# Performance work log

Measured on AMD Instinct MI355X. Metric: run time of the kernel, lower is better.

The kernel has to match this reference:

```python
import jax, jax.numpy as jnp
import numpy as np

N_HEAD = 16
NEG_INF = -1e30


def sparsemax(z):
    # sparsemax over last axis (Martins & Astudillo 2016)
    d = z.shape[-1]
    z_sorted = -jnp.sort(-z, axis=-1)                      # descending
    z_cumsum = jnp.cumsum(z_sorted, axis=-1)
    k = jnp.arange(1, d + 1, dtype=z.dtype)
    support = (1.0 + k * z_sorted) > z_cumsum
    rho = jnp.sum(support, axis=-1, keepdims=True)         # int, >=1
    rho_idx = jnp.clip(rho - 1, 0, None).astype(jnp.int32)
    cs_at_rho = jnp.take_along_axis(z_cumsum, rho_idx, axis=-1)
    tau = (cs_at_rho - 1.0) / jnp.maximum(rho.astype(z.dtype), 1.0)
    return jnp.clip(z - tau, 0.0, None)


def setup_inputs() -> dict:
    key = jax.random.key(0)
    ks = jax.random.split(key, 5)
    B, T, C = 4, 2048, 1024
    x = jax.random.normal(ks[0], (B, T, C), dtype=jnp.float32)
    W_attn = jax.random.normal(ks[1], (C, 3 * C), dtype=jnp.float32) * (1.0 / np.sqrt(C))
    b_attn = jax.random.normal(ks[2], (3 * C,), dtype=jnp.float32) * 0.01
    W_proj = jax.random.normal(ks[3], (C, C), dtype=jnp.float32) * (1.0 / np.sqrt(C))
    b_proj = jax.random.normal(ks[4], (C,), dtype=jnp.float32) * 0.01
    return {"x": x, "W_attn": W_attn, "b_attn": b_attn, "W_proj": W_proj, "b_proj": b_proj}


def reference(x, W_attn, b_attn, W_proj, b_proj):
    B, T, C = x.shape
    H = N_HEAD
    D = C // H
    qkv = x @ W_attn + b_attn                               # [B,T,3C]
    q, k, v = jnp.split(qkv, 3, axis=-1)
    q = q.reshape(B, T, H, D).transpose(0, 2, 1, 3)         # [B,H,T,D]
    k = k.reshape(B, T, H, D).transpose(0, 2, 1, 3)
    v = v.reshape(B, T, H, D).transpose(0, 2, 1, 3)
    # sparsemax over head dim of K (mode xsa_sparsemax_k)
    k = sparsemax(k)
    att = jnp.einsum('bhqd,bhkd->bhqk', q, k) * (1.0 / np.sqrt(D))
    causal = jnp.tril(jnp.ones((T, T), dtype=bool))
    att = jnp.where(causal[None, None], att, NEG_INF)
    att = jax.nn.softmax(att, axis=-1)
    y = jnp.einsum('bhqk,bhkd->bhqd', att, v)               # [B,H,T,D]
    # XSA output correction: subtract projection of y onto normalized v
    v_norm = jnp.sqrt(jnp.sum(v * v, axis=-1, keepdims=True))
    v_hat = v / jnp.maximum(v_norm, 1e-12)
    proj_coef = jnp.sum(y * v_hat, axis=-1, keepdims=True)
    y = y - proj_coef * v_hat
    y = y.transpose(0, 2, 1, 3).reshape(B, T, C)
    return y @ W_proj + b_proj
```

## Files before the change

### kernel.cpp

```cpp
#include <hip/hip_runtime.h>
#include <math.h>

#define NB 4
#define NH 16
#define TT 2048
#define CC 1024
#define DD 64
#define MM (NB * TT)
#define BK 32

typedef __attribute__((ext_vector_type(8))) _Float16 half8;
typedef __attribute__((ext_vector_type(4))) _Float16 half4;
typedef __attribute__((ext_vector_type(4))) float floatx4;

__device__ __forceinline__ void gload16(const _Float16* g, _Float16* l) {
    auto gp = (const __attribute__((address_space(1))) void*)(uintptr_t)g;
    auto lp = (__attribute__((address_space(3))) void*)(uint32_t)(uintptr_t)l;
    __builtin_amdgcn_global_load_lds(gp, lp, 16, 0, 0);
}

__global__ __launch_bounds__(256) void split_x_kernel(
    const float* __restrict__ x, _Float16* __restrict__ xh,
    _Float16* __restrict__ xl)
{
    size_t i = ((size_t)blockIdx.x * 256 + threadIdx.x) * 4;
    float4 v = *(const float4*)&x[i];
    half4 h, l;
    h.x = (_Float16)v.x; l.x = (_Float16)(v.x - (float)h.x);
    h.y = (_Float16)v.y; l.y = (_Float16)(v.y - (float)h.y);
    h.z = (_Float16)v.z; l.z = (_Float16)(v.z - (float)h.z);
    h.w = (_Float16)v.w; l.w = (_Float16)(v.w - (float)h.w);
    *(half4*)&xh[i] = h;
    *(half4*)&xl[i] = l;
}

__global__ __launch_bounds__(256) void splitT_w_kernel(
    const float* __restrict__ W, _Float16* __restrict__ WhT,
    _Float16* __restrict__ WlT, int K, int N)
{
    __shared__ float Ls[64][65];
    const int bN = blockIdx.x * 64;
    const int bK = blockIdx.y * 64;
    const int tid = threadIdx.x;
    const int g = tid >> 4, c = tid & 15;

    #pragma unroll
    for (int u = 0; u < 4; u++) {
        int r = u * 16 + g;
        float4 v = *(const float4*)&W[(size_t)(bK + r) * N + bN + c * 4];
        Ls[r][c * 4 + 0] = v.x; Ls[r][c * 4 + 1] = v.y;
        Ls[r][c * 4 + 2] = v.z; Ls[r][c * 4 + 3] = v.w;
    }
    __syncthreads();
    #pragma unroll
    for (int u = 0; u < 4; u++) {
        int n = u * 16 + g;
        half4 h, l;
        float f;
        f = Ls[c * 4 + 0][n]; h.x = (_Float16)f; l.x = (_Float16)(f - (float)h.x);
        f = Ls[c * 4 + 1][n]; h.y = (_Float16)f; l.y = (_Float16)(f - (float)h.y);
        f = Ls[c * 4 + 2][n]; h.z = (_Float16)f; l.z = (_Float16)(f - (float)h.z);
        f = Ls[c * 4 + 3][n]; h.w = (_Float16)f; l.w = (_Float16)(f - (float)h.w);
        size_t o = (size_t)(bN + n) * K + bK + c * 4;
        *(half4*)&WhT[o] = h;
        *(half4*)&WlT[o] = l;
    }
}

__global__ __launch_bounds__(512, 2) void gemm_ht3_kernel(
    const _Float16* __restrict__ Ah, const _Float16* __restrict__ Al,
    const _Float16* __restrict__ Bh, const _Float16* __restrict__ Bl,
    const float* __restrict__ bias, float* __restrict__ Cout,
    _Float16* __restrict__ outQh, _Float16* __restrict__ outQl,
    _Float16* __restrict__ outKh, _Float16* __restrict__ outKl,
    _Float16* __restrict__ outVt, int N, int K, int nbx, int mode)
{
    __shared__ _Float16 sAh[2][128 * BK], sAl[2][128 * BK];
    __shared__ _Float16 sBh[2][256 * BK], sBl[2][256 * BK];

    const int nblk = gridDim.x;
    const int id = blockIdx.x;
    const int swzid = (id & 7) * (nblk >> 3) + (id >> 3);
    const int by = swzid / nbx, bx = swzid - by * nbx;
    const int bm = by * 128, bn = bx * 256;

    const int tid = threadIdx.x;
    const int w = tid >> 6, lane = tid & 63;
    const int wm = (w >> 2) * 64, wn = (w & 3) * 64;
    const int fr = lane & 15, g = lane >> 4;

    const int rS = w * 16 + (lane >> 2);
    const int ug = ((lane & 3) ^ ((rS >> 1) & 3)) * 8;
    const size_t gA  = (size_t)(bm + rS) * K + ug;
    const size_t gB0 = (size_t)(bn + rS) * K + ug;
    const size_t gB1 = (size_t)(bn + 128 + rS) * K + ug;
    const int ldsW = w * 16 * BK;

    auto stage = [&](int kt, int c) {
        const int k0 = kt * BK;
        gload16(&Ah[gA + k0],  &sAh[c][ldsW]);
        gload16(&Al[gA + k0],  &sAl[c][ldsW]);
        gload16(&Bh[gB0 + k0], &sBh[c][ldsW]);
        gload16(&Bl[gB0 + k0], &sBl[c][ldsW]);
        gload16(&Bh[gB1 + k0], &sBh[c][128 * BK + ldsW]);
        gload16(&Bl[gB1 + k0], &sBl[c][128 * BK + ldsW]);
    };

    int offA[4], offB[4];
    #pragma unroll
    for (int t = 0; t < 4; t++) {
        const int ra = wm + t * 16 + fr;
        offA[t] = ra * BK + ((g ^ ((ra >> 1) & 3)) << 3);
        const int rb = wn + t * 16 + fr;
        offB[t] = rb * BK + ((g ^ ((rb >> 1) & 3)) << 3);
    }

    floatx4 acc[4][4];
    #pragma unroll
    for (int i = 0; i < 4; i++)
        #pragma unroll
        for (int j = 0; j < 4; j++)
            acc[i][j] = (floatx4){0.f, 0.f, 0.f, 0.f};

    stage(0, 0);
    stage(1, 1);
    __syncthreads();

    const int NK = K >> 5;
    for (int kt = 0; kt < NK; kt++) {
        const int c = kt & 1;
        half8 a_h[4], a_l[4], b_h[4], b_l[4];
        #pragma unroll
        for (int t = 0; t < 4; t++) {
            a_h[t] = *(const half8*)&sAh[c][offA[t]];
            a_l[t] = *(const half8*)&sAl[c][offA[t]];
            b_h[t] = *(const half8*)&sBh[c][offB[t]];
            b_l[t] = *(const half8*)&sBl[c][offB[t]];
        }
        __builtin_amdgcn_s_setprio(1);
        #pragma unroll
        for (int mt = 0; mt < 4; mt++)
            #pragma unroll
            for (int nt = 0; nt < 4; nt++) {
                acc[mt][nt] = __builtin_amdgcn_mfma_f32_16x16x32_f16(
                    a_h[mt], b_h[nt], acc[mt][nt], 0, 0, 0);
                acc[mt][nt] = __builtin_amdgcn_mfma_f32_16x16x32_f16(
                    a_h[mt], b_l[nt], acc[mt][nt], 0, 0, 0);
                acc[mt][nt] = __builtin_amdgcn_mfma_f32_16x16x32_f16(
                    a_l[mt], b_h[nt], acc[mt][nt], 0, 0, 0);
            }
        __builtin_amdgcn_s_setprio(0);
        __syncthreads();
        if (kt + 2 < NK) stage(kt + 2, c);
    }

    const int col = lane & 15, row4 = g * 4;
    if (mode == 0) {
        #pragma unroll
        for (int mt = 0; mt < 4; mt++)
            #pragma unroll
            for (int nt = 0; nt < 4; nt++) {
                const int n = bn + wn + nt * 16 + col;
                const float bv = bias[n];
                const int m0 = bm + wm + mt * 16 + row4;
                #pragma unroll
                for (int r = 0; r < 4; r++)
                    Cout[(size_t)(m0 + r) * N + n] = acc[mt][nt][r] + bv;
            }
    } else {
        #pragma unroll
        for (int mt = 0; mt < 4; mt++)
            #pragma unroll
            for (int nt = 0; nt < 4; nt++) {
                const int n = bn + wn + nt * 16 + col;
                const int which = n >> 10;
                const int cc_ = n & 1023;
                const int hh_ = cc_ >> 6, d = cc_ & 63;
                const int m0 = bm + wm + mt * 16 + row4;
                const int b = m0 >> 11, t0 = m0 & 2047;
                const size_t bhx = (size_t)b * NH + hh_;
                const float bv = bias[n];
                if (which == 0) {
                    #pragma unroll
                    for (int r = 0; r < 4; r++) {
                        const float qv = (acc[mt][nt][r] + bv) * 0.125f;
                        const _Float16 qh_ = (_Float16)qv;
                        const size_t o = (bhx * TT + t0 + r) * DD + d;
                        outQh[o] = qh_;
                        outQl[o] = (_Float16)(qv - (float)qh_);
                    }
                } else if (which == 1) {
                    #pragma unroll
                    for (int r = 0; r < 4; r++) {
                        const float kv = acc[mt][nt][r] + bv;
                        const _Float16 kh_ = (_Float16)kv;
                        const size_t o = (bhx * TT + t0 + r) * DD + d;
                        outKh[o] = kh_;
                        outKl[o] = (_Float16)(kv - (float)kh_);
                    }
                } else {
                    half4 vv;
                    #pragma unroll
                    for (int r = 0; r < 4; r++)
                        vv[r] = (_Float16)(acc[mt][nt][r] + bv);
                    *(half4*)&outVt[(bhx * DD + d) * TT + t0] = vv;
                }
            }
    }
}

__global__ __launch_bounds__(256) void sparsemax_kernel(
    _Float16* __restrict__ Kh, _Float16* __restrict__ Kl)
{
    const int lane = threadIdx.x & 63;
    const size_t row = (size_t)blockIdx.x * 4 + (threadIdx.x >> 6);
    const size_t off = row * DD + lane;
    float z = (float)Kh[off] + (float)Kl[off];
    float cnt = 0.f, ss = 0.f;
    #pragma unroll
    for (int j = 0; j < 64; j++) {
        float zj = __shfl(z, j, 64);
        if (zj >= z) { cnt += 1.f; ss += zj; }
    }
    float cond = (1.f + cnt * z > ss) ? 1.f : 0.f;
    float rho = cond, S = cond * z;
    #pragma unroll
    for (int o = 32; o; o >>= 1) {
        rho += __shfl_xor(rho, o, 64);
        S   += __shfl_xor(S,   o, 64);
    }
    float tau = (S - 1.f) / rho;
    float outv = fmaxf(z - tau, 0.f);
    _Float16 hh = (_Float16)outv;
    Kh[off] = hh;
    Kl[off] = (_Float16)(outv - (float)hh);
}

__global__ __launch_bounds__(256, 2) void attn_kernel(
    const _Float16* __restrict__ Qh, const _Float16* __restrict__ Ql,
    const _Float16* __restrict__ Kh, const _Float16* __restrict__ Kl,
    const _Float16* __restrict__ Vt,
    _Float16* __restrict__ Yh, _Float16* __restrict__ Yl)
{
    __shared__ _Float16 sKh[2][64 * DD];
    __shared__ _Float16 sKl[2][64 * DD];
    __shared__ _Float16 sV [2][64 * DD];

    const int tid = threadIdx.x;
    const int w = tid >> 6, lane = tid & 63;
    const int p = blockIdx.x >> 6;
    const int bhid = blockIdx.x & 63;
    const int b = bhid >> 4, h = bhid & 15;
    const size_t bh = (size_t)b * NH + h;
    const _Float16* Qhg = Qh + bh * (size_t)TT * DD;
    const _Float16* Qlg = Ql + bh * (size_t)TT * DD;
    const _Float16* Khg = Kh + bh * (size_t)TT * DD;
    const _Float16* Klg = Kl + bh * (size_t)TT * DD;
    const _Float16* Vtg = Vt + bh * (size_t)DD * TT;

    const int qrow = lane & 15;
    const int g = lane >> 4;
    const int swz = qrow & 7;
    const int sr = lane >> 3;
    const int uu = (lane & 7) ^ sr;

    auto stage = [&](int kt, int buf) {
        const int rb = w * 16;
        #pragma unroll
        for (int i = 0; i < 2; i++) {
            const int rr = rb + i * 8 + sr;
            const size_t ko = (size_t)(kt * 64 + rr) * DD + (uu << 3);
            gload16(&Khg[ko], &sKh[buf][(rb + i * 8) * DD]);
            gload16(&Klg[ko], &sKl[buf][(rb + i * 8) * DD]);
            gload16(&Vtg[(size_t)rr * TT + kt * 64 + (uu << 3)],
                    &sV[buf][(rb + i * 8) * DD]);
        }
    };

    const int qlist[2] = {p, 15 - p};
    int cur = 0;

    for (int qi = 0; qi < 2; qi++) {
        const int qt = qlist[qi];
        const int wq0 = qt * 128 + w * 32;
        const int wqmax = wq0 + 31;
        const int nkv = 2 * qt + 2;

        half8 qfh[2][2], qfl[2][2];
        #pragma unroll
        for (int nq = 0; nq < 2; nq++)
            #pragma unroll
            for (int ks = 0; ks < 2; ks++) {
                const size_t o = (size_t)(wq0 + nq * 16 + qrow) * DD
                               + (g << 3) + (ks << 5);
                qfh[nq][ks] = *(const half8*)&Qhg[o];
                qfl[nq][ks] = *(const half8*)&Qlg[o];
            }

        floatx4 acc[2][4];
        #pragma unroll
        for (int i = 0; i < 2; i++)
            #pragma unroll
            for (int j = 0; j < 4; j++)
                acc[i][j] = (floatx4){0.f, 0.f, 0.f, 0.f};
        float m_i[2] = {-3.0e38f, -3.0e38f};
        float l_i[2] = {0.f, 0.f};

        __syncthreads();
        stage(0, cur);

        for (int kt = 0; kt < nkv; kt++) {
            __syncthreads();
            if (kt + 1 < nkv) stage(kt + 1, cur ^ 1);

            if (kt * 64 <= wqmax) {
                const _Float16* kb = sKh[cur];
                const _Float16* lb = sKl[cur];
                const _Float16* vbp = sV[cur];

                floatx4 s[4][2];
                #pragma unroll
                for (int mk = 0; mk < 4; mk++)
                    #pragma unroll
                    for (int nq = 0; nq < 2; nq++)
                        s[mk][nq] = (floatx4){0.f, 0.f, 0.f, 0.f};

                #pragma unroll
                for (int mk = 0; mk < 4; mk++) {
                    #pragma unroll
                    for (int ks = 0; ks < 2; ks++) {
                        const int off = (qrow + mk * 16) * DD
                                      + (((g + (ks << 2)) ^ swz) << 3);
                        const half8 kfh = *(const half8*)&kb[off];
                        const half8 kfl = *(const half8*)&lb[off];
                        #pragma unroll
                        for (int nq = 0; nq < 2; nq++) {
                            s[mk][nq] = __builtin_amdgcn_mfma_f32_16x16x32_f16(
                                kfh, qfh[nq][ks], s[mk][nq], 0, 0, 0);
                            s[mk][nq] = __builtin_amdgcn_mfma_f32_16x16x32_f16(
                                kfh, qfl[nq][ks], s[mk][nq], 0, 0, 0);
                            s[mk][nq] = __builtin_amdgcn_mfma_f32_16x16x32_f16(
                                kfl, qfh[nq][ks], s[mk][nq], 0, 0, 0);
                        }
                    }
                }

                if (kt * 64 + 63 > wq0) {
                    #pragma unroll
                    for (int mk = 0; mk < 4; mk++)
                        #pragma unroll
                        for (int nq = 0; nq < 2; nq++)
                            #pragma unroll
                            for (int r = 0; r < 4; r++) {
                                const int kvg = kt * 64 + mk * 16 + (g << 2) + r;
                                const int qg  = wq0 + nq * 16 + qrow;
                                if (kvg > qg) s[mk][nq][r] = -1.0e30f;
                            }
                }

                float al_[2];
                #pragma unroll
                for (int nq = 0; nq < 2; nq++) {
                    float mx = s[0][nq][0];
                    #pragma unroll
                    for (int mk = 0; mk < 4; mk++)
                        #pragma unroll
                        for (int r = 0; r < 4; r++)
                            mx = fmaxf(mx, s[mk][nq][r]);
                    mx = fmaxf(mx, __shfl_xor(mx, 16, 64));
                    mx = fmaxf(mx, __shfl_xor(mx, 32, 64));
                    const float mn = fmaxf(m_i[nq], mx);
                    al_[nq] = __expf(m_i[nq] - mn);
                    m_i[nq] = mn;
                    float r0 = 0.f;
                    #pragma unroll
                    for (int mk = 0; mk < 4; mk++)
                        #pragma unroll
                        for (int r = 0; r < 4; r++) {
                            const float pp = __expf(s[mk][nq][r] - mn);
                            s[mk][nq][r] = pp;
                            r0 += pp;
                        }
                    r0 += __shfl_xor(r0, 16, 64);
                    r0 += __shfl_xor(r0, 32, 64);
                    l_i[nq] = l_i[nq] * al_[nq] + r0;
                }

                #pragma unroll
                for (int mt = 0; mt < 2; mt++)
                    #pragma unroll
                    for (int r = 0; r < 4; r++) {
                        const float aB = __shfl(al_[mt], (g << 2) | r, 64);
                        #pragma unroll
                        for (int nt = 0; nt < 4; nt++)
                            acc[mt][nt][r] *= aB;
                    }

                half4 ph[4][2], pl[4][2];
                #pragma unroll
                for (int mk = 0; mk < 4; mk++)
                    #pragma unroll
                    for (int nq = 0; nq < 2; nq++)
                        #pragma unroll
                        for (int r = 0; r < 4; r++) {
                            const float pv = s[mk][nq][r];
                            const _Float16 hh = (_Float16)pv;
                            ph[mk][nq][r] = hh;
                            pl[mk][nq][r] = (_Float16)(pv - (float)hh);
                        }

                #pragma unroll
                for (int mk = 0; mk < 4; mk++) {
                    #pragma unroll
                    for (int nt = 0; nt < 4; nt++) {
                        const int d = qrow + nt * 16;
                        const int u = ((mk << 1) | (g >> 1)) ^ swz;
                        const half4 vb = *(const half4*)
                            &vbp[d * DD + (u << 3) + ((g & 1) << 2)];
                        #pragma unroll
                        for (int nq = 0; nq < 2; nq++) {
                            acc[nq][nt] = __builtin_amdgcn_mfma_f32_16x16x16f16(
                                ph[mk][nq], vb, acc[nq][nt], 0, 0, 0);
                            acc[nq][nt] = __builtin_amdgcn_mfma_f32_16x16x16f16(
                                pl[mk][nq], vb, acc[nq][nt], 0, 0, 0);
                        }
                    }
                }
            }
            cur ^= 1;
        }

        #pragma unroll
        for (int mt = 0; mt < 2; mt++)
            #pragma unroll
            for (int r = 0; r < 4; r++) {
                const int qg = wq0 + mt * 16 + (g << 2) + r;
                const float invl = 1.0f / __shfl(l_i[mt], (g << 2) | r, 64);
                float y0 = acc[mt][0][r] * invl;
                float y1 = acc[mt][1][r] * invl;
                float y2 = acc[mt][2][r] * invl;
                float y3 = acc[mt][3][r] * invl;
                const float v0 = (float)Vtg[(size_t)qrow * TT + qg];
                const float v1 = (float)Vtg[(size_t)(qrow + 16) * TT + qg];
                const float v2 = (float)Vtg[(size_t)(qrow + 32) * TT + qg];
                const float v3 = (float)Vtg[(size_t)(qrow + 48) * TT + qg];
                float n2 = v0 * v0 + v1 * v1 + v2 * v2 + v3 * v3;
                #pragma unroll
                for (int o = 8; o; o >>= 1) n2 += __shfl_xor(n2, o, 64);
                const float ivn = 1.0f / fmaxf(sqrtf(n2), 1e-12f);
                float coef = y0 * v0 + y1 * v1 + y2 * v2 + y3 * v3;
                #pragma unroll
                for (int o = 8; o; o >>= 1) coef += __shfl_xor(coef, o, 64);
                coef *= ivn * ivn;
                const float o0 = y0 - coef * v0;
                const float o1 = y1 - coef * v1;
                const float o2 = y2 - coef * v2;
                const float o3 = y3 - coef * v3;
                const size_t ob = ((size_t)(b * TT + qg)) * CC + h * DD + qrow;
                _Float16 hh;
                hh = (_Float16)o0; Yh[ob]      = hh; Yl[ob]      = (_Float16)(o0 - (float)hh);
                hh = (_Float16)o1; Yh[ob + 16] = hh; Yl[ob + 16] = (_Float16)(o1 - (float)hh);
                hh = (_Float16)o2; Yh[ob + 32] = hh; Yl[ob + 32] = (_Float16)(o2 - (float)hh);
                hh = (_Float16)o3; Yh[ob + 48] = hh; Yl[ob + 48] = (_Float16)(o3 - (float)hh);
            }
    }
}

extern "C" void kernel_launch(void* const* d_in, const int* in_sizes, int n_in,
                              void* d_out, int out_size, void* d_ws, size_t ws_size,
                              hipStream_t stream) {
    const float* x      = (const float*)d_in[0];
    const float* W_attn = (const float*)d_in[1];
    const float* b_attn = (const float*)d_in[2];
    const float* W_proj = (const float*)d_in[3];
    const float* b_proj = (const float*)d_in[4];
    float* out = (float*)d_out;

    char* ws = (char*)d_ws;
    _Float16* xh   = (_Float16*)(ws);
    _Float16* xl   = (_Float16*)(ws + ((size_t)16 << 20));
    _Float16* WhT  = (_Float16*)(ws + ((size_t)32 << 20));
    _Float16* WlT  = (_Float16*)(ws + ((size_t)38 << 20));
    _Float16* Qh_  = (_Float16*)(ws + ((size_t)44 << 20));
    _Float16* Ql_  = (_Float16*)(ws + ((size_t)60 << 20));
    _Float16* Kh_  = (_Float16*)(ws + ((size_t)76 << 20));
    _Float16* Kl_  = (_Float16*)(ws + ((size_t)92 << 20));
    _Float16* Vt_  = (_Float16*)(ws + ((size_t)108 << 20));
    _Float16* Yh   = xh;
    _Float16* Yl   = xl;
    _Float16* WphT = WhT;
    _Float16* WplT = (_Float16*)(ws + ((size_t)34 << 20));

    split_x_kernel<<<(MM * CC) / (256 * 4), 256, 0, stream>>>(x, xh, xl);
    splitT_w_kernel<<<dim3(3 * CC / 64, CC / 64), 256, 0, stream>>>(
        W_attn, WhT, WlT, CC, 3 * CC);
    gemm_ht3_kernel<<<dim3((MM / 128) * (3 * CC / 256)), 512, 0, stream>>>(
        xh, xl, WhT, WlT, b_attn, nullptr,
        Qh_, Ql_, Kh_, Kl_, Vt_, 3 * CC, CC, 3 * CC / 256, 1);
    sparsemax_kernel<<<dim3((NB * NH * TT) / 4), 256, 0, stream>>>(Kh_, Kl_);
    attn_kernel<<<dim3(512), 256, 0, stream>>>(Qh_, Ql_, Kh_, Kl_, Vt_, Yh, Yl);
    splitT_w_kernel<<<dim3(CC / 64, CC / 64), 256, 0, stream>>>(
        W_proj, WphT, WplT, CC, CC);
    gemm_ht3_kernel<<<dim3((MM / 128) * (CC / 256)), 512, 0, stream>>>(
        Yh, Yl, WphT, WplT, b_proj, out,
        nullptr, nullptr, nullptr, nullptr, nullptr, CC, CC, CC / 256, 0);
}
```

Baseline: 541.1 us.

## Load low-half GEMM operands directly from global memory, halving LDS staging

The split-fp16 GEMM now stages only the high halves of A and B through LDS. The low halves are read straight from global memory into registers each k-step, and the occupancy hint rises from 2 to 4 blocks per CU. The three MFMA passes are also regrouped so each pass runs over all tiles before the next. This halves LDS footprint and the async-copy traffic, which should allow more resident blocks. In exchange, direct global loads sit on the critical path without prefetch and may stall the MFMA stream, and the tighter register limit may cause spills.

```diff
diff --git a/kernel.cpp b/kernel.cpp
--- a/kernel.cpp
+++ b/kernel.cpp
@@ -67,7 +67,7 @@
     }
 }
 
-__global__ __launch_bounds__(512, 2) void gemm_ht3_kernel(
+__global__ __launch_bounds__(512, 4) void gemm_ht3_kernel(
     const _Float16* __restrict__ Ah, const _Float16* __restrict__ Al,
     const _Float16* __restrict__ Bh, const _Float16* __restrict__ Bl,
     const float* __restrict__ bias, float* __restrict__ Cout,
@@ -75,8 +75,8 @@
     _Float16* __restrict__ outKh, _Float16* __restrict__ outKl,
     _Float16* __restrict__ outVt, int N, int K, int nbx, int mode)
 {
-    __shared__ _Float16 sAh[2][128 * BK], sAl[2][128 * BK];
-    __shared__ _Float16 sBh[2][256 * BK], sBl[2][256 * BK];
+    __shared__ _Float16 sAh[2][128 * BK];
+    __shared__ _Float16 sBh[2][256 * BK];
 
     const int nblk = gridDim.x;
     const int id = blockIdx.x;
@@ -99,20 +99,20 @@
     auto stage = [&](int kt, int c) {
         const int k0 = kt * BK;
         gload16(&Ah[gA + k0],  &sAh[c][ldsW]);
-        gload16(&Al[gA + k0],  &sAl[c][ldsW]);
         gload16(&Bh[gB0 + k0], &sBh[c][ldsW]);
-        gload16(&Bl[gB0 + k0], &sBl[c][ldsW]);
         gload16(&Bh[gB1 + k0], &sBh[c][128 * BK + ldsW]);
-        gload16(&Bl[gB1 + k0], &sBl[c][128 * BK + ldsW]);
     };
 
     int offA[4], offB[4];
+    size_t goA[4], goB[4];
     #pragma unroll
     for (int t = 0; t < 4; t++) {
         const int ra = wm + t * 16 + fr;
         offA[t] = ra * BK + ((g ^ ((ra >> 1) & 3)) << 3);
+        goA[t] = (size_t)(bm + ra) * K + (g << 3);
         const int rb = wn + t * 16 + fr;
         offB[t] = rb * BK + ((g ^ ((rb >> 1) & 3)) << 3);
+        goB[t] = (size_t)(bn + rb) * K + (g << 3);
     }
 
     floatx4 acc[4][4];
@@ -129,26 +129,38 @@
     const int NK = K >> 5;
     for (int kt = 0; kt < NK; kt++) {
         const int c = kt & 1;
-        half8 a_h[4], a_l[4], b_h[4], b_l[4];
+        const int k0 = kt * BK;
+        half8 a_l[4], b_l[4];
+        #pragma unroll
+        for (int t = 0; t < 4; t++) {
+            a_l[t] = *(const half8*)&Al[goA[t] + k0];
+            b_l[t] = *(const half8*)&Bl[goB[t] + k0];
+        }
+        half8 a_h[4], b_h[4];
         #pragma unroll
         for (int t = 0; t < 4; t++) {
             a_h[t] = *(const half8*)&sAh[c][offA[t]];
-            a_l[t] = *(const half8*)&sAl[c][offA[t]];
             b_h[t] = *(const half8*)&sBh[c][offB[t]];
-            b_l[t] = *(const half8*)&sBl[c][offB[t]];
         }
         __builtin_amdgcn_s_setprio(1);
         #pragma unroll
         for (int mt = 0; mt < 4; mt++)
             #pragma unroll
-            for (int nt = 0; nt < 4; nt++) {
+            for (int nt = 0; nt < 4; nt++)
                 acc[mt][nt] = __builtin_amdgcn_mfma_f32_16x16x32_f16(
                     a_h[mt], b_h[nt], acc[mt][nt], 0, 0, 0);
+        #pragma unroll
+        for (int mt = 0; mt < 4; mt++)
+            #pragma unroll
+            for (int nt = 0; nt < 4; nt++)
                 acc[mt][nt] = __builtin_amdgcn_mfma_f32_16x16x32_f16(
                     a_h[mt], b_l[nt], acc[mt][nt], 0, 0, 0);
+        #pragma unroll
+        for (int mt = 0; mt < 4; mt++)
+            #pragma unroll
+            for (int nt = 0; nt < 4; nt++)
                 acc[mt][nt] = __builtin_amdgcn_mfma_f32_16x16x32_f16(
                     a_l[mt], b_h[nt], acc[mt][nt], 0, 0, 0);
-            }
         __builtin_amdgcn_s_setprio(0);
         __syncthreads();
         if (kt + 2 < NK) stage(kt + 2, c);
```

New measurement: 920.3 us. 1.7x slower.
